# Performance work log

Hardware: AMD Instinct MI355X
Metric: run time of the kernel (lower is better)

## Reference

```python
import jax, jax.numpy as jnp
import numpy as np

B, S, D = 16, 4096, 64
SCALE = float(np.sqrt(D))  # sqrt(hidden_size)


def setup_inputs() -> dict:
    key = jax.random.key(0)
    kq, kk, kv = jax.random.split(key, 3)
    return {
        "query": jax.random.normal(kq, (B, S, D), dtype=jnp.float32),
        "key": jax.random.normal(kk, (B, S, D), dtype=jnp.float32),
        "value": jax.random.normal(kv, (B, S, D), dtype=jnp.float32),
    }


def reference(query, key, value):
    # energy: [B, S, S]
    energy = jnp.einsum("bqd,bkd->bqk", query, key) / SCALE
    attention = jax.nn.softmax(energy, axis=2)
    return jnp.einsum("bqk,bkd->bqd", attention, value)
```

## Files before the change

kernel.cpp:

```cpp
#include <hip/hip_runtime.h>


#define NBATCH 16
#define SEQ    4096
#define DIM    64
#define BQ     256
#define BK     64
#define NKT    (SEQ / BK)
#define KHALF  (NKT / 2)
#define OELEMS (NBATCH * SEQ * DIM)
#define NROWS  (NBATCH * SEQ)

#define QSCALE 0.180336879f

typedef _Float16 half4_t __attribute__((ext_vector_type(4)));
typedef _Float16 half8_t __attribute__((ext_vector_type(8)));
typedef float    floatx4 __attribute__((ext_vector_type(4)));

__device__ inline float fast_exp2(float x) {
#if __has_builtin(__builtin_amdgcn_exp2f)
  return __builtin_amdgcn_exp2f(x);
#else
  return exp2f(x);
#endif
}
__device__ inline float fast_rcp(float x) {
#if __has_builtin(__builtin_amdgcn_rcpf)
  return __builtin_amdgcn_rcpf(x);
#else
  return 1.0f / x;
#endif
}

__device__ inline int swz(int row, int col) {
  return row * 64 + ((((col >> 3) ^ ((row >> 1) & 7)) << 3) | (col & 7));
}

__global__ __launch_bounds__(256, 2)
void attn_f16_flash(const float* __restrict__ Qg, const float* __restrict__ Kg,
                    const float* __restrict__ Vg, float* __restrict__ O0g,
                    float* __restrict__ O1g, float* __restrict__ lsg)
{
  __shared__ __align__(16) _Float16 sK[64 * 64];
  __shared__ __align__(16) _Float16 sV[64 * 64];
  __shared__ __align__(16) _Float16 sP[4 * 64 * 64];

  const int tid  = threadIdx.x;
  const int wave = tid >> 6;
  const int lane = tid & 63;
  const int l16  = lane & 15;
  const int quad = lane >> 4;
  const int hK   = (l16 >> 1) & 7;

  const int t16 = tid & 15;
  const int kg  = tid >> 4;

  const int bid  = blockIdx.x;
  const int half = bid & 1;
  const int qb   = bid >> 1;
  const int b    = qb >> 4;
  const int qt   = qb & 15;
  const int q0   = qt * BQ + wave * 64;
  const int kt0  = half * KHALF;

  const float* Qb = Qg + ((size_t)b * SEQ + q0) * DIM;
  const float* Kb = Kg + (size_t)b * SEQ * DIM;
  const float* Vb = Vg + (size_t)b * SEQ * DIM;
  float*       Ob = (half ? O1g : O0g) + ((size_t)b * SEQ + q0) * DIM;
  float*       Ls = lsg + half * NROWS + b * SEQ + q0;

  half8_t qf[4][2];
  #pragma unroll
  for (int s = 0; s < 4; ++s)
    #pragma unroll
    for (int c = 0; c < 2; ++c) {
      const floatx4 f0 = *(const floatx4*)(Qb + (s * 16 + l16) * DIM + c * 32 + quad * 8);
      const floatx4 f1 = *(const floatx4*)(Qb + (s * 16 + l16) * DIM + c * 32 + quad * 8 + 4);
      half8_t h;
      #pragma unroll
      for (int j = 0; j < 4; ++j) h[j] = (_Float16)(f0[j] * QSCALE);
      #pragma unroll
      for (int j = 0; j < 4; ++j) h[4 + j] = (_Float16)(f1[j] * QSCALE);
      qf[s][c] = h;
    }

  floatx4 oacc[4][4];
  float   lsum[4][4];
  #pragma unroll
  for (int s = 0; s < 4; ++s) {
    #pragma unroll
    for (int n = 0; n < 4; ++n) oacc[s][n] = (floatx4){0.f, 0.f, 0.f, 0.f};
    #pragma unroll
    for (int r = 0; r < 4; ++r) lsum[s][r] = 0.f;
  }

  _Float16* myP = &sP[wave * 64 * 64];

  floatx4 kbuf[4], vbuf[4];

  #define LOAD_TILE(KT)                                                        \
    do {                                                                       \
      const float* Kt_ = Kb + (size_t)(KT) * BK * DIM;                         \
      const float* Vt_ = Vb + (size_t)(KT) * BK * DIM;                         \
      _Pragma("unroll")                                                        \
      for (int i = 0; i < 4; ++i) {                                            \
        const int key = kg + 16 * i;                                           \
        kbuf[i] = *(const floatx4*)(Kt_ + key * DIM + t16 * 4);                \
        vbuf[i] = *(const floatx4*)(Vt_ + key * DIM + t16 * 4);                \
      }                                                                        \
    } while (0)

  #define WRITE_TILE()                                                         \
    do {                                                                       \
      _Pragma("unroll")                                                        \
      for (int i = 0; i < 4; ++i) {             \
        const int key = kg + 16 * i;                                           \
        half4_t h;                                                             \
        _Pragma("unroll")                                                      \
        for (int j = 0; j < 4; ++j) h[j] = (_Float16)kbuf[i][j];               \
        *(half4_t*)&sK[swz(key, t16 * 4)] = h;                                 \
      }                                                                        \
      _Pragma("unroll")                                                        \
      for (int e = 0; e < 4; ++e) {             \
        const int dim = t16 * 4 + e;                                           \
        half4_t h;                                                             \
        _Pragma("unroll")                                                      \
        for (int i = 0; i < 4; ++i) h[i] = (_Float16)vbuf[i][e];               \
        *(half4_t*)&sV[swz(dim, kg * 4)] = h;                                  \
      }                                                                        \
    } while (0)

  #define QK_EXP()                                                             \
    do {                                                                       \
      floatx4 sc[4][4];                                                        \
      _Pragma("unroll")                                                        \
      for (int s = 0; s < 4; ++s)                                              \
        _Pragma("unroll")                                                      \
        for (int n = 0; n < 4; ++n) sc[s][n] = (floatx4){0.f, 0.f, 0.f, 0.f};  \
      _Pragma("unroll")                                                        \
      for (int n = 0; n < 4; ++n)                                              \
        _Pragma("unroll")                                                      \
        for (int c = 0; c < 2; ++c) {                                          \
          half8_t bf = *(const half8_t*)&sK[(n * 16 + l16) * 64 +              \
                                            (((c * 4 + quad) ^ hK) << 3)];     \
          _Pragma("unroll")                                                    \
          for (int s = 0; s < 4; ++s)                                          \
            sc[s][n] = __builtin_amdgcn_mfma_f32_16x16x32_f16(qf[s][c], bf,    \
                                                              sc[s][n], 0, 0, 0);\
        }                                                                      \
      _Pragma("unroll")                                                        \
      for (int s = 0; s < 4; ++s)                                              \
        _Pragma("unroll")                                                      \
        for (int r = 0; r < 4; ++r) {                                          \
          const int prow = s * 16 + quad * 4 + r;                              \
          half4_t ph;                                                          \
          _Pragma("unroll")                                                    \
          for (int n = 0; n < 4; ++n) {                                        \
            float p = fast_exp2(sc[s][n][r]);                                  \
            lsum[s][r] += p;                                                   \
            ph[n] = (_Float16)p;                                               \
          }                                                                    \
          *(half4_t*)&myP[swz(prow, l16 * 4)] = ph;                            \
        }                                                                      \
    } while (0)

  #define PV()                                                                 \
    do {                                                                       \
      _Pragma("unroll")                                                        \
      for (int c = 0; c < 2; ++c) {                                            \
        half8_t pf[4];                                                         \
        _Pragma("unroll")                                                      \
        for (int s = 0; s < 4; ++s)                                            \
          pf[s] = *(const half8_t*)&myP[(s * 16 + l16) * 64 +                  \
                                        (((c * 4 + quad) ^ hK) << 3)];         \
        _Pragma("unroll")                                                      \
        for (int n = 0; n < 4; ++n) {                                          \
          half8_t vf = *(const half8_t*)&sV[(n * 16 + l16) * 64 +              \
                                            (((c * 4 + quad) ^ hK) << 3)];     \
          _Pragma("unroll")                                                    \
          for (int s = 0; s < 4; ++s)                                          \
            oacc[s][n] = __builtin_amdgcn_mfma_f32_16x16x32_f16(pf[s], vf,     \
                                                                oacc[s][n], 0, 0, 0);\
        }                                                                      \
      }                                                                        \
    } while (0)

  LOAD_TILE(kt0);
  WRITE_TILE();
  __syncthreads();

  #pragma unroll 1
  for (int kt = kt0; kt < kt0 + KHALF - 1; ++kt) {
    LOAD_TILE(kt + 1);
    QK_EXP();
    PV();
    __syncthreads();
    WRITE_TILE();
    __syncthreads();
  }
  QK_EXP();
  PV();

  #pragma unroll
  for (int s = 0; s < 4; ++s) {
    float rsum[4];
    #pragma unroll
    for (int r = 0; r < 4; ++r) {
      float v = lsum[s][r];
      v += __shfl_xor(v, 1);
      v += __shfl_xor(v, 2);
      v += __shfl_xor(v, 4);
      v += __shfl_xor(v, 8);
      rsum[r] = v;
    }
    if (l16 == 0) {
      #pragma unroll
      for (int r = 0; r < 4; ++r)
        Ls[s * 16 + quad * 4 + r] = rsum[r];
    }
    #pragma unroll
    for (int n = 0; n < 4; ++n)
      #pragma unroll
      for (int r = 0; r < 4; ++r)
        Ob[(s * 16 + quad * 4 + r) * DIM + n * 16 + l16] = oacc[s][n][r];
  }
  #undef LOAD_TILE
  #undef WRITE_TILE
  #undef QK_EXP
  #undef PV
}

__global__ __launch_bounds__(256)
void attn_combine(float* __restrict__ O, const float* __restrict__ O1,
                  const float* __restrict__ lsg)
{
  const int i = blockIdx.x * 256 + threadIdx.x;
  const float* l0 = lsg;
  const float* l1 = lsg + NROWS;
  const int row = i >> 4;
  const float inv = fast_rcp(l0[row] + l1[row]);
  const float4 a  = ((const float4*)O)[i];
  const float4 bb = ((const float4*)O1)[i];
  float4 r;
  r.x = (a.x + bb.x) * inv;
  r.y = (a.y + bb.y) * inv;
  r.z = (a.z + bb.z) * inv;
  r.w = (a.w + bb.w) * inv;
  ((float4*)O)[i] = r;
}

extern "C" void kernel_launch(void* const* d_in, const int* in_sizes, int n_in,
                              void* d_out, int out_size, void* d_ws, size_t ws_size,
                              hipStream_t stream) {
  const float* Q = (const float*)d_in[0];
  const float* K = (const float*)d_in[1];
  const float* V = (const float*)d_in[2];
  float* O  = (float*)d_out;
  float* O1 = (float*)d_ws;
  float* Ls = (float*)d_ws + OELEMS;
  (void)in_sizes; (void)n_in; (void)out_size; (void)ws_size;

  attn_f16_flash<<<dim3(2 * NBATCH * (SEQ / BQ)), dim3(256), 0, stream>>>(Q, K, V, O, O1, Ls);
  attn_combine<<<dim3(OELEMS / 4 / 256), dim3(256), 0, stream>>>(O, O1, Ls);
}
```

Baseline: 190.5 us.

## Keep softmax probabilities in registers by computing transposed S^T and O^T

```diff
diff --git a/kernel.cpp b/kernel.cpp
--- a/kernel.cpp
+++ b/kernel.cpp
@@ -13,6 +13,7 @@
 
 #define QSCALE 0.180336879f
 
+typedef _Float16 half2_t __attribute__((ext_vector_type(2)));
 typedef _Float16 half4_t __attribute__((ext_vector_type(4)));
 typedef _Float16 half8_t __attribute__((ext_vector_type(8)));
 typedef float    floatx4 __attribute__((ext_vector_type(4)));
@@ -43,7 +44,6 @@
 {
   __shared__ __align__(16) _Float16 sK[64 * 64];
   __shared__ __align__(16) _Float16 sV[64 * 64];
-  __shared__ __align__(16) _Float16 sP[4 * 64 * 64];
 
   const int tid  = threadIdx.x;
   const int wave = tid >> 6;
@@ -84,17 +84,14 @@
       qf[s][c] = h;
     }
 
-  floatx4 oacc[4][4];
-  float   lsum[4][4];
-  #pragma unroll
-  for (int s = 0; s < 4; ++s) {
+  floatx4 oacc2[4][4];
+  float   lsum2[4];
+  #pragma unroll
+  for (int n = 0; n < 4; ++n)
     #pragma unroll
-    for (int n = 0; n < 4; ++n) oacc[s][n] = (floatx4){0.f, 0.f, 0.f, 0.f};
-    #pragma unroll
-    for (int r = 0; r < 4; ++r) lsum[s][r] = 0.f;
-  }
-
-  _Float16* myP = &sP[wave * 64 * 64];
+    for (int s = 0; s < 4; ++s) oacc2[n][s] = (floatx4){0.f, 0.f, 0.f, 0.f};
+  #pragma unroll
+  for (int s = 0; s < 4; ++s) lsum2[s] = 0.f;
 
   floatx4 kbuf[4], vbuf[4];
 
@@ -113,76 +110,72 @@
   #define WRITE_TILE()                                                         \
     do {                                                                       \
       _Pragma("unroll")                                                        \
-      for (int i = 0; i < 4; ++i) {             \
+      for (int i = 0; i < 4; ++i) {                                            \
         const int key = kg + 16 * i;                                           \
         half4_t h;                                                             \
         _Pragma("unroll")                                                      \
         for (int j = 0; j < 4; ++j) h[j] = (_Float16)kbuf[i][j];               \
         *(half4_t*)&sK[swz(key, t16 * 4)] = h;                                 \
       }                                                                        \
-      _Pragma("unroll")                                                        \
-      for (int e = 0; e < 4; ++e) {             \
-        const int dim = t16 * 4 + e;                                           \
-        half4_t h;                                                             \
-        _Pragma("unroll")                                                      \
-        for (int i = 0; i < 4; ++i) h[i] = (_Float16)vbuf[i][e];               \
-        *(half4_t*)&sV[swz(dim, kg * 4)] = h;                                  \
+      {                                                                        \
+        const int vbase = (kg >> 2) * 8 + (kg & 3) * 2;                        \
+        _Pragma("unroll")                                                      \
+        for (int e = 0; e < 4; ++e) {                                          \
+          const int dim = t16 * 4 + e;                                         \
+          half2_t h0; h0[0] = (_Float16)vbuf[0][e]; h0[1] = (_Float16)vbuf[1][e];\
+          half2_t h1; h1[0] = (_Float16)vbuf[2][e]; h1[1] = (_Float16)vbuf[3][e];\
+          *(half2_t*)&sV[swz(dim, vbase)]      = h0;                           \
+          *(half2_t*)&sV[swz(dim, vbase + 32)] = h1;                           \
+        }                                                                      \
       }                                                                        \
     } while (0)
 
-  #define QK_EXP()                                                             \
+  #define COMPUTE_TILE()                                                       \
     do {                                                                       \
-      floatx4 sc[4][4];                                                        \
-      _Pragma("unroll")                                                        \
-      for (int s = 0; s < 4; ++s)                                              \
-        _Pragma("unroll")                                                      \
-        for (int n = 0; n < 4; ++n) sc[s][n] = (floatx4){0.f, 0.f, 0.f, 0.f};  \
-      _Pragma("unroll")                                                        \
-      for (int n = 0; n < 4; ++n)                                              \
+      floatx4 sc[4][4];                           \
+      _Pragma("unroll")                                                        \
+      for (int nk = 0; nk < 4; ++nk)                                           \
+        _Pragma("unroll")                                                      \
+        for (int s = 0; s < 4; ++s) sc[nk][s] = (floatx4){0.f, 0.f, 0.f, 0.f}; \
+                         \
+      _Pragma("unroll")                                                        \
+      for (int nk = 0; nk < 4; ++nk)                                           \
         _Pragma("unroll")                                                      \
         for (int c = 0; c < 2; ++c) {                                          \
-          half8_t bf = *(const half8_t*)&sK[(n * 16 + l16) * 64 +              \
+          half8_t kf = *(const half8_t*)&sK[(nk * 16 + l16) * 64 +             \
                                             (((c * 4 + quad) ^ hK) << 3)];     \
           _Pragma("unroll")                                                    \
           for (int s = 0; s < 4; ++s)                                          \
-            sc[s][n] = __builtin_amdgcn_mfma_f32_16x16x32_f16(qf[s][c], bf,    \
-                                                              sc[s][n], 0, 0, 0);\
-        }                                                                      \
+            sc[nk][s] = __builtin_amdgcn_mfma_f32_16x16x32_f16(kf, qf[s][c],   \
+                                                               sc[nk][s], 0, 0, 0);\
+        }                                                                      \
+              \
+      half8_t bfrag[4][2];                                                     \
       _Pragma("unroll")                                                        \
       for (int s = 0; s < 4; ++s)                                              \
         _Pragma("unroll")                                                      \
-        for (int r = 0; r < 4; ++r) {                                          \
-          const int prow = s * 16 + quad * 4 + r;                              \
-          half4_t ph;                                                          \
+        for (int c = 0; c < 2; ++c) {                                          \
+          half8_t bf;                                                          \
           _Pragma("unroll")                                                    \
-          for (int n = 0; n < 4; ++n) {                                        \
-            float p = fast_exp2(sc[s][n][r]);                                  \
-            lsum[s][r] += p;                                                   \
-            ph[n] = (_Float16)p;                                               \
+          for (int j = 0; j < 8; ++j) {                                        \
+            float p = fast_exp2(sc[(c << 1) | (j & 1)][s][j >> 1]);            \
+            lsum2[s] += p;                                                     \
+            bf[j] = (_Float16)p;                                               \
           }                                                                    \
-          *(half4_t*)&myP[swz(prow, l16 * 4)] = ph;                            \
-        }                                                                      \
-    } while (0)
-
-  #define PV()                                                                 \
-    do {                                                                       \
-      _Pragma("unroll")                                                        \
-      for (int c = 0; c < 2; ++c) {                                            \
-        half8_t pf[4];                                                         \
-        _Pragma("unroll")                                                      \
-        for (int s = 0; s < 4; ++s)                                            \
-          pf[s] = *(const half8_t*)&myP[(s * 16 + l16) * 64 +                  \
-                                        (((c * 4 + quad) ^ hK) << 3)];         \
+          bfrag[s][c] = bf;                                                    \
+        }                                                                      \
+                  \
+      _Pragma("unroll")                                                        \
+      for (int c = 0; c < 2; ++c)                                              \
         _Pragma("unroll")                                                      \
         for (int n = 0; n < 4; ++n) {                                          \
           half8_t vf = *(const half8_t*)&sV[(n * 16 + l16) * 64 +              \
                                             (((c * 4 + quad) ^ hK) << 3)];     \
           _Pragma("unroll")                                                    \
           for (int s = 0; s < 4; ++s)                                          \
-            oacc[s][n] = __builtin_amdgcn_mfma_f32_16x16x32_f16(pf[s], vf,     \
-                                                                oacc[s][n], 0, 0, 0);\
-        }                                                                      \
-      }                                                                        \
+            oacc2[n][s] = __builtin_amdgcn_mfma_f32_16x16x32_f16(vf, bfrag[s][c],\
+                                                                 oacc2[n][s], 0, 0, 0);\
+        }                                                                      \
     } while (0)
 
   LOAD_TILE(kt0);
@@ -192,42 +185,29 @@
   #pragma unroll 1
   for (int kt = kt0; kt < kt0 + KHALF - 1; ++kt) {
     LOAD_TILE(kt + 1);
-    QK_EXP();
-    PV();
+    COMPUTE_TILE();
     __syncthreads();
     WRITE_TILE();
     __syncthreads();
   }
-  QK_EXP();
-  PV();
+  COMPUTE_TILE();
 
   #pragma unroll
   for (int s = 0; s < 4; ++s) {
-    float rsum[4];
-    #pragma unroll
-    for (int r = 0; r < 4; ++r) {
-      float v = lsum[s][r];
-      v += __shfl_xor(v, 1);
-      v += __shfl_xor(v, 2);
-      v += __shfl_xor(v, 4);
-      v += __shfl_xor(v, 8);
-      rsum[r] = v;
-    }
-    if (l16 == 0) {
-      #pragma unroll
-      for (int r = 0; r < 4; ++r)
-        Ls[s * 16 + quad * 4 + r] = rsum[r];
-    }
+    float v = lsum2[s];
+    v += __shfl_xor(v, 16);
+    v += __shfl_xor(v, 32);
+    if (lane < 16) Ls[s * 16 + l16] = v;
+  }
+  #pragma unroll
+  for (int s = 0; s < 4; ++s)
     #pragma unroll
     for (int n = 0; n < 4; ++n)
-      #pragma unroll
-      for (int r = 0; r < 4; ++r)
-        Ob[(s * 16 + quad * 4 + r) * DIM + n * 16 + l16] = oacc[s][n][r];
-  }
+      *(floatx4*)&Ob[(s * 16 + l16) * DIM + n * 16 + quad * 4] = oacc2[n][s];
+
   #undef LOAD_TILE
   #undef WRITE_TILE
-  #undef QK_EXP
-  #undef PV
+  #undef COMPUTE_TILE
 }
 
 __global__ __launch_bounds__(256)
```

Measured after the change: 168.4 us. -11.6%, faster.
